# Kernel optimization log

Hardware: AMD Instinct MI355X
Metric: run time of the kernel (lower is better)

The kernel has to match this reference:

```python
import jax, jax.numpy as jnp
import numpy as np

CHAR_DIM = 96
COLOR_DIM = 16
GLYPH_DIM = CHAR_DIM * COLOR_DIM  # 1536 bounded id space
CHAR_EMB = 16
COLOR_EMB = 4
GLYPH_EMB = CHAR_EMB + COLOR_EMB  # 20
HID = 32
MAX_LEN = 64


def setup_inputs() -> dict:
    key = jax.random.key(0)
    ks = jax.random.split(key, 8)
    B, H, W = 4096, 21, 79
    glyph_chars = jax.random.randint(ks[0], (B, H, W), 0, CHAR_DIM)
    glyph_colors = jax.random.randint(ks[1], (B, H, W), 0, COLOR_DIM)
    # embedding tables (row CHAR_DIM / COLOR_DIM is the padding row)
    char_table = jax.random.normal(ks[2], (CHAR_DIM + 1, CHAR_EMB), jnp.float32) * 0.1
    col_table = jax.random.normal(ks[3], (COLOR_DIM + 1, COLOR_EMB), jnp.float32) * 0.1
    s = 1.0 / np.sqrt(HID)
    Wih = jax.random.uniform(ks[4], (HID, GLYPH_EMB), jnp.float32, -s, s)
    Whh = jax.random.uniform(ks[5], (HID, HID), jnp.float32, -s, s)
    bih = jax.random.uniform(ks[6], (HID,), jnp.float32, -s, s)
    bhh = jax.random.uniform(ks[7], (HID,), jnp.float32, -s, s)
    return dict(glyph_chars=glyph_chars, glyph_colors=glyph_colors,
                char_table=char_table, col_table=col_table,
                Wih=Wih, Whh=Whh, bih=bih, bhh=bhh)


def reference(glyph_chars, glyph_colors, char_table, col_table, Wih, Whh, bih, bhh):
    B = glyph_chars.shape[0]
    # combined glyph id in the bounded [0, GLYPH_DIM) space
    ids = (glyph_chars * COLOR_DIM + glyph_colors).reshape(B, -1)  # [B, H*W]
    # batched fixed-size histogram over the bounded id space (replaces per-sample torch.unique)
    counts = jnp.zeros((B, GLYPH_DIM), jnp.int32).at[jnp.arange(B)[:, None], ids].add(1)
    present = counts > 0  # [B, GLYPH_DIM]
    # sorted unique ids (ascending == lexicographic over (char,color)); absent ids pushed to GLYPH_DIM
    sorted_ids = jnp.sort(jnp.where(present, jnp.arange(GLYPH_DIM), GLYPH_DIM), axis=-1)[:, :MAX_LEN]
    is_pad = sorted_ids >= GLYPH_DIM
    char_bag = jnp.where(is_pad, CHAR_DIM, sorted_ids // COLOR_DIM)   # pad -> CHAR_DIM row
    color_bag = jnp.where(is_pad, COLOR_DIM, sorted_ids % COLOR_DIM)  # pad -> COLOR_DIM row
    bag = jnp.stack([char_bag, color_bag], axis=-1)  # [B, MAX_LEN, 2]
    lengths = jnp.minimum(present.sum(-1), MAX_LEN)  # [B]
    emb = jnp.concatenate([char_table[char_bag], col_table[color_bag]], axis=-1)  # [B, MAX_LEN, 20]
    # vanilla tanh RNN over the packed (variable-length) bag; keep hidden at last valid step
    def step(h, inp):
        x_t, t = inp  # x_t: [B, 20]
        h_new = jnp.tanh(x_t @ Wih.T + bih + h @ Whh.T + bhh)
        h = jnp.where((t < lengths)[:, None], h_new, h)
        return h, None
    h0 = jnp.zeros((B, HID), emb.dtype)
    h, _ = jax.lax.scan(step, h0, (emb.transpose(1, 0, 2), jnp.arange(MAX_LEN)))
    return h, emb, bag
```

## Files before the change

kernel.cpp:

```cpp
#include <hip/hip_runtime.h>
#include <hip/hip_bf16.h>

#define HW        1659
#define GLYPH_DIM 1536

typedef _Float16 half8  __attribute__((ext_vector_type(8)));
typedef _Float16 half2v __attribute__((ext_vector_type(2)));
typedef float    f32x4  __attribute__((ext_vector_type(4)));

__device__ __forceinline__ float tanh_f(float x) {
    float e = __expf(x + x);
    return fmaf(-2.0f, __builtin_amdgcn_rcpf(e + 1.0f), 1.0f);
}

__device__ __forceinline__ unsigned int pk(float a, float b) {
    return __builtin_bit_cast(unsigned int, __builtin_amdgcn_cvt_pkrtz(a, b));
}

__device__ __forceinline__ half8 h8(unsigned int a, unsigned int b,
                                    unsigned int c, unsigned int d) {
    uint4 u = make_uint4(a, b, c, d);
    return __builtin_bit_cast(half8, u);
}

__global__ __launch_bounds__(256, 8) void k1_histo(
    const int* __restrict__ gchar, const int* __restrict__ gcol,
    unsigned short* __restrict__ ids_bt,
    unsigned short* __restrict__ ids_tb,
    int* __restrict__ lens_g)
{
    __shared__ unsigned int   mask[4][48];
    __shared__ unsigned short ids_s[4][64];

    const int tid = threadIdx.x;
    const int b0  = blockIdx.x * 4;

    if (tid < 192) ((unsigned int*)mask)[tid] = 0u;
    __syncthreads();

    const int4* cp = (const int4*)(gchar + (long)b0 * HW);
    const int4* kp = (const int4*)(gcol  + (long)b0 * HW);
    const int n4 = HW;
    int idx = tid;
    bool valid = idx < n4;
    int4 c = {}, k = {};
    if (valid) { c = cp[idx]; k = kp[idx]; }
    while (valid) {
        int  idx1 = idx + 256;
        bool v1   = idx1 < n4;
        int4 c1 = {}, k1 = {};
        if (v1) { c1 = cp[idx1]; k1 = kp[idx1]; }
        {
            int gg  = idx * 4;
            int bl0 = gg / HW;
            int rem = gg - bl0 * HW;
            int bl1 = bl0 + ((rem + 1) >= HW);
            int bl2 = bl0 + ((rem + 2) >= HW);
            int bl3 = bl0 + ((rem + 3) >= HW);
            int id0 = c.x * 16 + k.x;
            int id1 = c.y * 16 + k.y;
            int id2 = c.z * 16 + k.z;
            int id3 = c.w * 16 + k.w;
            atomicOr(&mask[bl0][id0 >> 5], 1u << (id0 & 31));
            atomicOr(&mask[bl1][id1 >> 5], 1u << (id1 & 31));
            atomicOr(&mask[bl2][id2 >> 5], 1u << (id2 & 31));
            atomicOr(&mask[bl3][id3 >> 5], 1u << (id3 & 31));
        }
        idx = idx1; valid = v1; c = c1; k = k1;
    }
    __syncthreads();

    if (tid < 128) {
        const int bl  = tid >> 5;
        const int l32 = tid & 31;
        unsigned long long m = 0ull;
        if (l32 < 24)
            m = ((unsigned long long)mask[bl][2 * l32 + 1] << 32) |
                (unsigned long long)mask[bl][2 * l32];
        int cnt  = __popcll(m);
        int incl = cnt;
        #pragma unroll
        for (int d = 1; d < 32; d <<= 1) {
            int nb = __shfl_up(incl, d, 32);
            if (l32 >= d) incl += nb;
        }
        int excl  = incl - cnt;
        int total = __shfl(incl, 31, 32);
        if (l32 == 0) lens_g[b0 + bl] = min(total, 64);
        ids_s[bl][l32]      = GLYPH_DIM;
        ids_s[bl][l32 + 32] = GLYPH_DIM;
        unsigned long long mm = m;
        int r = excl;
        while (mm != 0ull && r < 64) {
            int bit = __builtin_ctzll(mm);
            ids_s[bl][r] = (unsigned short)(l32 * 64 + bit);
            ++r;
            mm &= (mm - 1ull);
        }
    }
    __syncthreads();

    if (tid < 128)
        ((unsigned int*)(ids_bt + (long)b0 * 64))[tid] = ((unsigned int*)ids_s)[tid];
    {
        const int bl = tid >> 6, t = tid & 63;
        const int b  = b0 + bl;
        ids_tb[((long)(b >> 6) * 64 + t) * 64 + (b & 63)] = ids_s[bl][t];
    }
}

__global__ __launch_bounds__(256, 4) void k23_main(
    const float* __restrict__ ctab, const float* __restrict__ ktab,
    const float* __restrict__ Wih, const float* __restrict__ Whh,
    const float* __restrict__ bih, const float* __restrict__ bhh,
    const unsigned short* __restrict__ ids_bt,
    const unsigned short* __restrict__ ids_tb,
    const int* __restrict__ lens_g,
    float* __restrict__ out_h, float* __restrict__ out_emb,
    float* __restrict__ out_bag, int nrnn)
{
    __shared__ float          tabs[1620];
    __shared__ unsigned short ids_t[64 * 64];

    const int tid = threadIdx.x;

    for (int i = tid; i < 1620; i += 256)
        tabs[i] = (i < 1552) ? ctab[i] : ktab[i - 1552];

    if ((int)blockIdx.x < nrnn) {
        {
            const unsigned int* src = (const unsigned int*)(ids_tb + (long)blockIdx.x * 4096);
            unsigned int* dst = (unsigned int*)ids_t;
            #pragma unroll
            for (int j = 0; j < 8; ++j) dst[tid + j * 256] = src[tid + j * 256];
        }
        const int n = tid & 15, g = (tid >> 4) & 3;
        half8 wihA0, wihA1, whhA0, whhA1;
        #pragma unroll
        for (int j = 0; j < 8; ++j) {
            int kk = (j < 4) ? (4 * g + j) : (12 + 4 * g + j);
            wihA0[j] = (_Float16)((kk < 20) ? Wih[n * 20 + kk] : 0.0f);
            wihA1[j] = (_Float16)((kk < 20) ? Wih[(n + 16) * 20 + kk] : 0.0f);
            whhA0[j] = (_Float16)Whh[n * 32 + kk];
            whhA1[j] = (_Float16)Whh[(n + 16) * 32 + kk];
        }
        f32x4 bias0, bias1;
        #pragma unroll
        for (int i = 0; i < 4; ++i) {
            bias0[i] = bih[4 * g + i] + bhh[4 * g + i];
            bias1[i] = bih[16 + 4 * g + i] + bhh[16 + 4 * g + i];
        }
        const int ib  = (tid >> 6) * 16 + n;
        const int b   = blockIdx.x * 64 + ib;
        const int len = lens_g[b];
        __syncthreads();

        auto build = [&](int id) -> half8 {
            int ch = id >> 4;
            int co = (id >= GLYPH_DIM) ? 16 : (id & 15);
            f32x4 q1 = *(const f32x4*)&tabs[ch * 16 + 4 * g];
            f32x4 q2 = {0.0f, 0.0f, 0.0f, 0.0f};
            if (g == 0) q2 = *(const f32x4*)&tabs[1552 + co * 4];
            return h8(pk(q1[0], q1[1]), pk(q1[2], q1[3]),
                      pk(q2[0], q2[1]), pk(q2[2], q2[3]));
        };

        half8 x0  = build(ids_t[0 * 64 + ib]);
        f32x4 Pc0 = __builtin_amdgcn_mfma_f32_16x16x32_f16(wihA0, x0, bias0, 0, 0, 0);
        f32x4 Pc1 = __builtin_amdgcn_mfma_f32_16x16x32_f16(wihA1, x0, bias1, 0, 0, 0);
        int   idn = ids_t[1 * 64 + ib];
        f32x4 d0 = {0, 0, 0, 0}, d1 = {0, 0, 0, 0};
        for (int t = 0; t < 64; ++t) {
            f32x4 Pn0 = Pc0, Pn1 = Pc1;
            int   id2 = (t < 62) ? (int)ids_t[(t + 2) * 64 + ib] : idn;
            if (t < 63) {
                half8 xn = build(idn);
                Pn0 = __builtin_amdgcn_mfma_f32_16x16x32_f16(wihA0, xn, bias0, 0, 0, 0);
                Pn1 = __builtin_amdgcn_mfma_f32_16x16x32_f16(wihA1, xn, bias1, 0, 0, 0);
            }
            half8 hB = h8(pk(d0[0], d0[1]), pk(d0[2], d0[3]),
                          pk(d1[0], d1[1]), pk(d1[2], d1[3]));
            f32x4 a0 = __builtin_amdgcn_mfma_f32_16x16x32_f16(whhA0, hB, Pc0, 0, 0, 0);
            f32x4 a1 = __builtin_amdgcn_mfma_f32_16x16x32_f16(whhA1, hB, Pc1, 0, 0, 0);
            bool upd = (t < len);
            #pragma unroll
            for (int i = 0; i < 4; ++i) {
                float h0 = tanh_f(a0[i]);
                float h1 = tanh_f(a1[i]);
                d0[i] = upd ? h0 : d0[i];
                d1[i] = upd ? h1 : d1[i];
            }
            Pc0 = Pn0; Pc1 = Pn1; idn = id2;
        }
        float* op = out_h + (long)b * 32;
        *(f32x4*)(op + 4 * g)      = d0;
        *(f32x4*)(op + 16 + 4 * g) = d1;
    } else {
        __syncthreads();
        const long row = (long)((int)blockIdx.x - nrnn) * 256 + tid;
        int id = ids_bt[row];
        int ch = id >> 4;
        int co = (id >= GLYPH_DIM) ? 16 : (id & 15);
        f32x4 c0 = *(const f32x4*)&tabs[ch * 16 + 0];
        f32x4 c1 = *(const f32x4*)&tabs[ch * 16 + 4];
        f32x4 c2 = *(const f32x4*)&tabs[ch * 16 + 8];
        f32x4 c3 = *(const f32x4*)&tabs[ch * 16 + 12];
        f32x4 k0 = *(const f32x4*)&tabs[1552 + co * 4];
        float* gp = out_emb + row * 20;
        *(f32x4*)(gp + 0)  = c0;
        *(f32x4*)(gp + 4)  = c1;
        *(f32x4*)(gp + 8)  = c2;
        *(f32x4*)(gp + 12) = c3;
        *(f32x4*)(gp + 16) = k0;
        *(float2*)(out_bag + row * 2) = make_float2((float)ch, (float)co);
    }
}

extern "C" void kernel_launch(void* const* d_in, const int* in_sizes, int n_in,
                              void* d_out, int out_size, void* d_ws, size_t ws_size,
                              hipStream_t stream) {
    const int* gchar = (const int*)d_in[0];
    const int* gcol  = (const int*)d_in[1];
    const float* ctab = (const float*)d_in[2];
    const float* ktab = (const float*)d_in[3];
    const float* Wih  = (const float*)d_in[4];
    const float* Whh  = (const float*)d_in[5];
    const float* bih  = (const float*)d_in[6];
    const float* bhh  = (const float*)d_in[7];

    const int B = in_sizes[0] / HW;
    float* out_h   = (float*)d_out;
    float* out_emb = out_h + (long)B * 32;
    float* out_bag = out_emb + (long)B * 64 * 20;

    unsigned short* ids_bt = (unsigned short*)d_ws;
    unsigned short* ids_tb = ids_bt + (long)B * 64;
    int*            lens_g = (int*)((char*)d_ws + (long)B * 64 * 4);

    k1_histo<<<B / 4, 256, 0, stream>>>(gchar, gcol, ids_bt, ids_tb, lens_g);

    const int nrnn = B / 64;
    const int nemb = (B * 64) / 256;
    k23_main<<<nrnn + nemb, 256, 0, stream>>>(
        ctab, ktab, Wih, Whh, bih, bhh, ids_bt, ids_tb, lens_g,
        out_h, out_emb, out_bag, nrnn);
}
```

Before: 45.78 us.

## Precompute input projections in parallel, run recurrence on one wave in fp16

Restructures the RNN blocks so each block handles 16 samples. All four waves first compute the input projections Wih·x+bias for the 64 timesteps and store them as packed fp16 in LDS. A single wave then runs the serial recurrence, using a packed-half Padé tanh approximation and carrying the hidden state in fp16. This takes the input-projection MFMAs and the embedding gathers off the serial critical path and spreads the RNN over four times as many blocks. The cost is lower precision in the hidden state and tanh, three idle waves during the recurrence, and lower occupancy from the larger LDS footprint (launch bounds drop to 2).

Measured after the change: 54.40 us. +18.8%, slower.

```diff
diff --git a/kernel.cpp b/kernel.cpp
--- a/kernel.cpp
+++ b/kernel.cpp
@@ -8,25 +8,50 @@
 typedef _Float16 half2v __attribute__((ext_vector_type(2)));
 typedef float    f32x4  __attribute__((ext_vector_type(4)));
 
-__device__ __forceinline__ float tanh_f(float x) {
-    float e = __expf(x + x);
-    return fmaf(-2.0f, __builtin_amdgcn_rcpf(e + 1.0f), 1.0f);
-}
-
 __device__ __forceinline__ unsigned int pk(float a, float b) {
     return __builtin_bit_cast(unsigned int, __builtin_amdgcn_cvt_pkrtz(a, b));
 }
 
-__device__ __forceinline__ half8 h8(unsigned int a, unsigned int b,
-                                    unsigned int c, unsigned int d) {
+__device__ __forceinline__ half8 h8u(unsigned int a, unsigned int b,
+                                     unsigned int c, unsigned int d) {
     uint4 u = make_uint4(a, b, c, d);
     return __builtin_bit_cast(half8, u);
+}
+
+__device__ __forceinline__ unsigned int tanh_pk(unsigned int w) {
+    const half2v hP4  = {(_Float16)4.0f,  (_Float16)4.0f};
+    const half2v hM4  = {(_Float16)-4.0f, (_Float16)-4.0f};
+    const half2v h105 = {(_Float16)105.0f, (_Float16)105.0f};
+    const half2v h945 = {(_Float16)945.0f, (_Float16)945.0f};
+    const half2v h15  = {(_Float16)15.0f,  (_Float16)15.0f};
+    const half2v h420 = {(_Float16)420.0f, (_Float16)420.0f};
+    const half2v hP1  = {(_Float16)1.0f,  (_Float16)1.0f};
+    const half2v hM1  = {(_Float16)-1.0f, (_Float16)-1.0f};
+    half2v x = __builtin_bit_cast(half2v, w);
+    x = __builtin_elementwise_max(__builtin_elementwise_min(x, hP4), hM4);
+    half2v y   = x * x;
+    half2v num = x * (y * (y + h105) + h945);
+    half2v den = y * (y * h15 + h420) + h945;
+    half2v r   = num / den;
+    r = __builtin_elementwise_max(__builtin_elementwise_min(r, hP1), hM1);
+    return __builtin_bit_cast(unsigned int, r);
+}
+
+__device__ __forceinline__ void unpack4(uint4 p, f32x4& c0, f32x4& c1) {
+    half2v a = __builtin_bit_cast(half2v, p.x);
+    half2v b = __builtin_bit_cast(half2v, p.y);
+    half2v c = __builtin_bit_cast(half2v, p.z);
+    half2v d = __builtin_bit_cast(half2v, p.w);
+    c0[0] = (float)a[0]; c0[1] = (float)a[1];
+    c0[2] = (float)b[0]; c0[3] = (float)b[1];
+    c1[0] = (float)c[0]; c1[1] = (float)c[1];
+    c1[2] = (float)d[0]; c1[3] = (float)d[1];
 }
 
 __global__ __launch_bounds__(256, 8) void k1_histo(
     const int* __restrict__ gchar, const int* __restrict__ gcol,
     unsigned short* __restrict__ ids_bt,
-    unsigned short* __restrict__ ids_tb,
+    unsigned short* __restrict__ ids_tb16,
     int* __restrict__ lens_g)
 {
     __shared__ unsigned int   mask[4][48];
@@ -105,97 +130,109 @@
     {
         const int bl = tid >> 6, t = tid & 63;
         const int b  = b0 + bl;
-        ids_tb[((long)(b >> 6) * 64 + t) * 64 + (b & 63)] = ids_s[bl][t];
-    }
-}
-
-__global__ __launch_bounds__(256, 4) void k23_main(
+        ids_tb16[((long)(b >> 4) * 64 + t) * 16 + (b & 15)] = ids_s[bl][t];
+    }
+}
+
+__global__ __launch_bounds__(256, 2) void k23_main(
     const float* __restrict__ ctab, const float* __restrict__ ktab,
     const float* __restrict__ Wih, const float* __restrict__ Whh,
     const float* __restrict__ bih, const float* __restrict__ bhh,
     const unsigned short* __restrict__ ids_bt,
-    const unsigned short* __restrict__ ids_tb,
+    const unsigned short* __restrict__ ids_tb16,
     const int* __restrict__ lens_g,
     float* __restrict__ out_h, float* __restrict__ out_emb,
     float* __restrict__ out_bag, int nrnn)
 {
-    __shared__ float          tabs[1620];
-    __shared__ unsigned short ids_t[64 * 64];
+    __shared__ __align__(16) uint4 P_lds[64 * 64];
+    __shared__ float tabs[1620];
 
     const int tid = threadIdx.x;
 
-    for (int i = tid; i < 1620; i += 256)
-        tabs[i] = (i < 1552) ? ctab[i] : ktab[i - 1552];
-
     if ((int)blockIdx.x < nrnn) {
-        {
-            const unsigned int* src = (const unsigned int*)(ids_tb + (long)blockIdx.x * 4096);
-            unsigned int* dst = (unsigned int*)ids_t;
-            #pragma unroll
-            for (int j = 0; j < 8; ++j) dst[tid + j * 256] = src[tid + j * 256];
-        }
-        const int n = tid & 15, g = (tid >> 4) & 3;
-        half8 wihA0, wihA1, whhA0, whhA1;
+        const int bg = blockIdx.x;
+        const int l  = tid & 63, w = tid >> 6;
+        const int n  = l & 15,  g = l >> 4;
+
+        half8 wihA0, wihA1;
+        f32x4 bias0, bias1;
         #pragma unroll
         for (int j = 0; j < 8; ++j) {
             int kk = (j < 4) ? (4 * g + j) : (12 + 4 * g + j);
             wihA0[j] = (_Float16)((kk < 20) ? Wih[n * 20 + kk] : 0.0f);
             wihA1[j] = (_Float16)((kk < 20) ? Wih[(n + 16) * 20 + kk] : 0.0f);
-            whhA0[j] = (_Float16)Whh[n * 32 + kk];
-            whhA1[j] = (_Float16)Whh[(n + 16) * 32 + kk];
-        }
-        f32x4 bias0, bias1;
+        }
         #pragma unroll
         for (int i = 0; i < 4; ++i) {
             bias0[i] = bih[4 * g + i] + bhh[4 * g + i];
             bias1[i] = bih[16 + 4 * g + i] + bhh[16 + 4 * g + i];
         }
-        const int ib  = (tid >> 6) * 16 + n;
-        const int b   = blockIdx.x * 64 + ib;
-        const int len = lens_g[b];
-        __syncthreads();
-
-        auto build = [&](int id) -> half8 {
+
+        const unsigned short* idp = ids_tb16 + (long)bg * 1024;
+        #pragma unroll 4
+        for (int tt = 0; tt < 16; ++tt) {
+            int t  = w * 16 + tt;
+            int id = idp[t * 16 + n];
             int ch = id >> 4;
             int co = (id >= GLYPH_DIM) ? 16 : (id & 15);
-            f32x4 q1 = *(const f32x4*)&tabs[ch * 16 + 4 * g];
+            f32x4 q1 = *(const f32x4*)(ctab + ch * 16 + 4 * g);
             f32x4 q2 = {0.0f, 0.0f, 0.0f, 0.0f};
-            if (g == 0) q2 = *(const f32x4*)&tabs[1552 + co * 4];
-            return h8(pk(q1[0], q1[1]), pk(q1[2], q1[3]),
-                      pk(q2[0], q2[1]), pk(q2[2], q2[3]));
-        };
-
-        half8 x0  = build(ids_t[0 * 64 + ib]);
-        f32x4 Pc0 = __builtin_amdgcn_mfma_f32_16x16x32_f16(wihA0, x0, bias0, 0, 0, 0);
-        f32x4 Pc1 = __builtin_amdgcn_mfma_f32_16x16x32_f16(wihA1, x0, bias1, 0, 0, 0);
-        int   idn = ids_t[1 * 64 + ib];
-        f32x4 d0 = {0, 0, 0, 0}, d1 = {0, 0, 0, 0};
-        for (int t = 0; t < 64; ++t) {
-            f32x4 Pn0 = Pc0, Pn1 = Pc1;
-            int   id2 = (t < 62) ? (int)ids_t[(t + 2) * 64 + ib] : idn;
-            if (t < 63) {
-                half8 xn = build(idn);
-                Pn0 = __builtin_amdgcn_mfma_f32_16x16x32_f16(wihA0, xn, bias0, 0, 0, 0);
-                Pn1 = __builtin_amdgcn_mfma_f32_16x16x32_f16(wihA1, xn, bias1, 0, 0, 0);
+            if (g == 0) q2 = *(const f32x4*)(ktab + co * 4);
+            half8 xB = h8u(pk(q1[0], q1[1]), pk(q1[2], q1[3]),
+                           pk(q2[0], q2[1]), pk(q2[2], q2[3]));
+            f32x4 P0 = __builtin_amdgcn_mfma_f32_16x16x32_f16(wihA0, xB, bias0, 0, 0, 0);
+            f32x4 P1 = __builtin_amdgcn_mfma_f32_16x16x32_f16(wihA1, xB, bias1, 0, 0, 0);
+            P_lds[t * 64 + l] = make_uint4(pk(P0[0], P0[1]), pk(P0[2], P0[3]),
+                                           pk(P1[0], P1[1]), pk(P1[2], P1[3]));
+        }
+        __syncthreads();
+
+        if (w == 0) {
+            half8 whhA0, whhA1;
+            #pragma unroll
+            for (int j = 0; j < 8; ++j) {
+                int kk = (j < 4) ? (4 * g + j) : (12 + 4 * g + j);
+                whhA0[j] = (_Float16)Whh[n * 32 + kk];
+                whhA1[j] = (_Float16)Whh[(n + 16) * 32 + kk];
             }
-            half8 hB = h8(pk(d0[0], d0[1]), pk(d0[2], d0[3]),
-                          pk(d1[0], d1[1]), pk(d1[2], d1[3]));
-            f32x4 a0 = __builtin_amdgcn_mfma_f32_16x16x32_f16(whhA0, hB, Pc0, 0, 0, 0);
-            f32x4 a1 = __builtin_amdgcn_mfma_f32_16x16x32_f16(whhA1, hB, Pc1, 0, 0, 0);
-            bool upd = (t < len);
-            #pragma unroll
-            for (int i = 0; i < 4; ++i) {
-                float h0 = tanh_f(a0[i]);
-                float h1 = tanh_f(a1[i]);
-                d0[i] = upd ? h0 : d0[i];
-                d1[i] = upd ? h1 : d1[i];
+            const int len = lens_g[bg * 16 + n];
+            unsigned int hw0 = 0u, hw1 = 0u, hw2 = 0u, hw3 = 0u;
+            uint4 pc = P_lds[l];
+            f32x4 cc0, cc1;
+            unpack4(pc, cc0, cc1);
+            for (int t = 0; t < 64; ++t) {
+                uint4 pn = P_lds[((t < 63) ? t + 1 : 63) * 64 + l];
+                half8 hB = h8u(hw0, hw1, hw2, hw3);
+                f32x4 a0 = __builtin_amdgcn_mfma_f32_16x16x32_f16(whhA0, hB, cc0, 0, 0, 0);
+                f32x4 a1 = __builtin_amdgcn_mfma_f32_16x16x32_f16(whhA1, hB, cc1, 0, 0, 0);
+                unpack4(pn, cc0, cc1);
+                unsigned int t0 = tanh_pk(pk(a0[0], a0[1]));
+                unsigned int t1 = tanh_pk(pk(a0[2], a0[3]));
+                unsigned int t2 = tanh_pk(pk(a1[0], a1[1]));
+                unsigned int t3 = tanh_pk(pk(a1[2], a1[3]));
+                bool upd = (t < len);
+                hw0 = upd ? t0 : hw0;
+                hw1 = upd ? t1 : hw1;
+                hw2 = upd ? t2 : hw2;
+                hw3 = upd ? t3 : hw3;
             }
-            Pc0 = Pn0; Pc1 = Pn1; idn = id2;
-        }
-        float* op = out_h + (long)b * 32;
-        *(f32x4*)(op + 4 * g)      = d0;
-        *(f32x4*)(op + 16 + 4 * g) = d1;
+            float* op = out_h + (long)(bg * 16 + n) * 32;
+            half2v u0 = __builtin_bit_cast(half2v, hw0);
+            half2v u1 = __builtin_bit_cast(half2v, hw1);
+            half2v u2 = __builtin_bit_cast(half2v, hw2);
+            half2v u3 = __builtin_bit_cast(half2v, hw3);
+            op[4 * g + 0]      = (float)u0[0];
+            op[4 * g + 1]      = (float)u0[1];
+            op[4 * g + 2]      = (float)u1[0];
+            op[4 * g + 3]      = (float)u1[1];
+            op[16 + 4 * g + 0] = (float)u2[0];
+            op[16 + 4 * g + 1] = (float)u2[1];
+            op[16 + 4 * g + 2] = (float)u3[0];
+            op[16 + 4 * g + 3] = (float)u3[1];
+        }
     } else {
+        for (int i = tid; i < 1620; i += 256)
+            tabs[i] = (i < 1552) ? ctab[i] : ktab[i - 1552];
         __syncthreads();
         const long row = (long)((int)blockIdx.x - nrnn) * 256 + tid;
         int id = ids_bt[row];
@@ -233,15 +270,15 @@
     float* out_emb = out_h + (long)B * 32;
     float* out_bag = out_emb + (long)B * 64 * 20;
 
-    unsigned short* ids_bt = (unsigned short*)d_ws;
-    unsigned short* ids_tb = ids_bt + (long)B * 64;
-    int*            lens_g = (int*)((char*)d_ws + (long)B * 64 * 4);
-
-    k1_histo<<<B / 4, 256, 0, stream>>>(gchar, gcol, ids_bt, ids_tb, lens_g);
-
-    const int nrnn = B / 64;
-    const int nemb = (B * 64) / 256;
+    unsigned short* ids_bt   = (unsigned short*)d_ws;
+    unsigned short* ids_tb16 = ids_bt + (long)B * 64;
+    int*            lens_g   = (int*)((char*)d_ws + (long)B * 64 * 4);
+
+    k1_histo<<<B / 4, 256, 0, stream>>>(gchar, gcol, ids_bt, ids_tb16, lens_g);
+
+    const int nrnn = B / 16;
+    const int nemb = B / 4;
     k23_main<<<nrnn + nemb, 256, 0, stream>>>(
-        ctab, ktab, Wih, Whh, bih, bhh, ids_bt, ids_tb, lens_g,
+        ctab, ktab, Wih, Whh, bih, bhh, ids_bt, ids_tb16, lens_g,
         out_h, out_emb, out_bag, nrnn);
 }
```
